# Kernel tuning notes

Measured on AMD Instinct MI355X. Metric: run time of the kernel, lower is better.

The kernel has to match this reference:

```python
import jax, jax.numpy as jnp
import numpy as np

B, L, D, H, UNITS = 64, 1024, 1024, 1024, 1024


def setup_inputs() -> dict:
    key = jax.random.key(0)
    ks = jax.random.split(key, 8)
    s = lambda fan_in: 1.0 / np.sqrt(fan_in)
    return {
        "features": jax.random.normal(ks[0], (B, L, D), jnp.float32),
        "hidden": jax.random.normal(ks[1], (B, H), jnp.float32),
        "W1": jax.random.normal(ks[2], (D, UNITS), jnp.float32) * s(D),
        "b1": jnp.zeros((UNITS,), jnp.float32),
        "W2": jax.random.normal(ks[3], (H, UNITS), jnp.float32) * s(H),
        "b2": jnp.zeros((UNITS,), jnp.float32),
        "V": jax.random.normal(ks[4], (UNITS, 1), jnp.float32) * s(UNITS),
        "bV": jnp.zeros((1,), jnp.float32),
    }


def reference(features, hidden, W1, b1, W2, b2, V, bV):
    # features: [B, L, D], hidden: [B, H]
    proj_f = jnp.einsum("bld,du->blu", features, W1) + b1          # [B, L, U]
    proj_h = (hidden @ W2 + b2)[:, None, :]                         # [B, 1, U]
    score = jnp.tanh(proj_f + proj_h)                               # [B, L, U]
    logits = jnp.einsum("blu,uo->blo", score, V) + bV               # [B, L, 1]
    attention_weights = jax.nn.softmax(logits, axis=1)              # [B, L, 1]
    context_vector = jnp.sum(attention_weights * features, axis=1)  # [B, D]
    return context_vector, attention_weights
```

## Files before the change

kernel.cpp:

```cpp
#include <hip/hip_runtime.h>
#include <hip/hip_bf16.h>
#include <stdint.h>

#define B_ 64
#define L_ 1024
#define D_ 1024
#define U_ 1024
#define M_ (B_ * L_)

typedef __attribute__((ext_vector_type(8))) __bf16 bf16x8;
typedef __attribute__((ext_vector_type(4))) float f32x4;

__device__ __forceinline__ unsigned short f2bf(float f) {
  unsigned u = __float_as_uint(f);
  unsigned r = (u + 0x7fffu + ((u >> 16) & 1u)) >> 16;
  return (unsigned short)r;
}

__device__ __forceinline__ void async_copy16(const void* gptr, void* ldsptr) {
  __builtin_amdgcn_global_load_lds(
      (const __attribute__((address_space(1))) void*)gptr,
      (__attribute__((address_space(3))) void*)ldsptr,
      16, 0, 0);
}

__global__ __launch_bounds__(256) void convert_f_bf16(
    const float4* __restrict__ src, ushort4* __restrict__ dst) {
  long i = (long)blockIdx.x * 256 + threadIdx.x;
  float4 v = src[i];
  ushort4 o;
  o.x = f2bf(v.x); o.y = f2bf(v.y); o.z = f2bf(v.z); o.w = f2bf(v.w);
  dst[i] = o;
}

__global__ __launch_bounds__(256) void transpose_w1(
    const float* __restrict__ W1, unsigned short* __restrict__ W1T) {
  __shared__ float tile[32][33];
  int tx = threadIdx.x & 31, ty = threadIdx.x >> 5;
  int u0 = blockIdx.x * 32, k0 = blockIdx.y * 32;
#pragma unroll
  for (int i = ty; i < 32; i += 8) tile[i][tx] = W1[(long)(k0 + i) * U_ + u0 + tx];
  __syncthreads();
#pragma unroll
  for (int i = ty; i < 32; i += 8)
    W1T[(long)(u0 + i) * D_ + k0 + tx] = f2bf(tile[tx][i]);
}

__global__ __launch_bounds__(256) void proj_h_kernel(
    const float* __restrict__ hidden, const float* __restrict__ W2,
    const float* __restrict__ b1, const float* __restrict__ b2,
    float* __restrict__ ph) {
  int u = blockIdx.x * 256 + threadIdx.x;
  int bbase = blockIdx.y * 8;
  int h0 = blockIdx.z * 512;
  float acc[8];
  float bias = (blockIdx.z == 0) ? (b1[u] + b2[u]) : 0.0f;
#pragma unroll
  for (int i = 0; i < 8; ++i) acc[i] = bias;
  for (int h = h0; h < h0 + 512; ++h) {
    float w = W2[(long)h * U_ + u];
#pragma unroll
    for (int i = 0; i < 8; ++i) acc[i] += hidden[(bbase + i) * 1024 + h] * w;
  }
#pragma unroll
  for (int i = 0; i < 8; ++i) atomicAdd(&ph[(bbase + i) * U_ + u], acc[i]);
}

__global__ __launch_bounds__(256, 2) void fused_score_kernel(
    const unsigned short* __restrict__ A,
    const unsigned short* __restrict__ Bt,
    const float* __restrict__ ph,
    const float* __restrict__ V,
    float* __restrict__ logits) {
  __shared__ unsigned short As[128 * 32];
  __shared__ unsigned short Bs[128 * 32];

  const int tid = threadIdx.x;
  const int wave = tid >> 6;
  const int lane = tid & 63;
  const int l15 = lane & 15;
  const int quad = lane >> 4;
  const int wm = wave >> 1;
  const int wn = wave & 1;
  const long m0 = (long)blockIdx.y * 128;
  const int n0 = blockIdx.x * 128;

  const int srow = lane >> 2;
  const int skof = (lane & 3) * 8;
  const int c0 = wave * 2;
  const unsigned short* Ab = A + (m0 + srow) * 1024 + skof;
  const unsigned short* Bb = Bt + ((long)n0 + srow) * 1024 + skof;

  f32x4 acc[4][4];
#pragma unroll
  for (int i = 0; i < 4; ++i)
#pragma unroll
    for (int j = 0; j < 4; ++j) acc[i][j] = (f32x4){0.f, 0.f, 0.f, 0.f};

  for (int k0 = 0; k0 < 1024; k0 += 32) {
#pragma unroll
    for (int cc = 0; cc < 2; ++cc) {
      const int c = c0 + cc;
      async_copy16(Ab + (long)c * 16 * 1024 + k0, &As[c * 512]);
      async_copy16(Bb + (long)c * 16 * 1024 + k0, &Bs[c * 512]);
    }
    __syncthreads();

    bf16x8 af[4], bf[4];
#pragma unroll
    for (int mi = 0; mi < 4; ++mi)
      af[mi] = *(const bf16x8*)&As[(wm * 64 + mi * 16 + l15) * 32 + quad * 8];
#pragma unroll
    for (int ni = 0; ni < 4; ++ni)
      bf[ni] = *(const bf16x8*)&Bs[(wn * 64 + ni * 16 + l15) * 32 + quad * 8];
#pragma unroll
    for (int mi = 0; mi < 4; ++mi)
#pragma unroll
      for (int ni = 0; ni < 4; ++ni)
        acc[mi][ni] = __builtin_amdgcn_mfma_f32_16x16x32_bf16(
            af[mi], bf[ni], acc[mi][ni], 0, 0, 0);
    __syncthreads();
  }

  const int b = (int)(m0 >> 10);
  float phv[4], vv[4];
#pragma unroll
  for (int ni = 0; ni < 4; ++ni) {
    int u = n0 + wn * 64 + ni * 16 + l15;
    phv[ni] = ph[b * U_ + u];
    vv[ni] = V[u];
  }
#pragma unroll
  for (int mi = 0; mi < 4; ++mi) {
#pragma unroll
    for (int r = 0; r < 4; ++r) {
      float part = 0.f;
#pragma unroll
      for (int ni = 0; ni < 4; ++ni) {
        float s = acc[mi][ni][r] + phv[ni];
        float t = __expf(2.0f * s);
        float th = 1.0f - 2.0f * __builtin_amdgcn_rcpf(t + 1.0f);
        part += th * vv[ni];
      }
      part += __shfl_xor(part, 1, 16);
      part += __shfl_xor(part, 2, 16);
      part += __shfl_xor(part, 4, 16);
      part += __shfl_xor(part, 8, 16);
      if (l15 == 0)
        atomicAdd(&logits[m0 + wm * 64 + mi * 16 + quad * 4 + r], part);
    }
  }
}

__global__ __launch_bounds__(256) void softmax_kernel(
    const float* __restrict__ logits, float* __restrict__ wout) {
  __shared__ float redm[4];
  __shared__ float reds[4];
  int b = blockIdx.x;
  int tid = threadIdx.x;
  int wave = tid >> 6, lane = tid & 63;
  float4 v = *(const float4*)&logits[b * 1024 + tid * 4];
  float m = fmaxf(fmaxf(v.x, v.y), fmaxf(v.z, v.w));
#pragma unroll
  for (int off = 32; off >= 1; off >>= 1) m = fmaxf(m, __shfl_xor(m, off, 64));
  if (lane == 0) redm[wave] = m;
  __syncthreads();
  m = fmaxf(fmaxf(redm[0], redm[1]), fmaxf(redm[2], redm[3]));
  float e0 = __expf(v.x - m), e1 = __expf(v.y - m);
  float e2 = __expf(v.z - m), e3 = __expf(v.w - m);
  float s = e0 + e1 + e2 + e3;
#pragma unroll
  for (int off = 32; off >= 1; off >>= 1) s += __shfl_xor(s, off, 64);
  if (lane == 0) reds[wave] = s;
  __syncthreads();
  s = reds[0] + reds[1] + reds[2] + reds[3];
  float inv = 1.0f / s;
  float4 o = {e0 * inv, e1 * inv, e2 * inv, e3 * inv};
  *(float4*)&wout[b * 1024 + tid * 4] = o;
}

__global__ __launch_bounds__(256) void context_kernel(
    const float* __restrict__ features, const float* __restrict__ wv,
    float* __restrict__ out) {
  int b = blockIdx.x;
  int d = blockIdx.y * 256 + threadIdx.x;
  int l0 = blockIdx.z * 128;
  const float* fp = features + ((long)b * 1024 + l0) * 1024 + d;
  const float* wp = wv + b * 1024 + l0;
  float acc = 0.f;
#pragma unroll 4
  for (int l = 0; l < 128; ++l) acc += wp[l] * fp[(long)l * 1024];
  atomicAdd(&out[b * 1024 + d], acc);
}

extern "C" void kernel_launch(void* const* d_in, const int* in_sizes, int n_in,
                              void* d_out, int out_size, void* d_ws, size_t ws_size,
                              hipStream_t stream) {
  const float* features = (const float*)d_in[0];
  const float* hidden   = (const float*)d_in[1];
  const float* W1       = (const float*)d_in[2];
  const float* b1       = (const float*)d_in[3];
  const float* W2       = (const float*)d_in[4];
  const float* b2       = (const float*)d_in[5];
  const float* V        = (const float*)d_in[6];

  char* ws = (char*)d_ws;
  unsigned short* Fh  = (unsigned short*)ws;
  unsigned short* W1T = (unsigned short*)(ws + 134217728);
  float* ph     = (float*)(ws + 134217728 + 2097152);
  float* logits = (float*)(ws + 134217728 + 2097152 + 262144);
  float* ctx  = (float*)d_out;
  float* wout = (float*)d_out + 65536;

  hipMemsetAsync(ph, 0, 262144 + 262144, stream);
  hipMemsetAsync(d_out, 0, 65536 * sizeof(float), stream);

  convert_f_bf16<<<65536, 256, 0, stream>>>((const float4*)features, (ushort4*)Fh);
  transpose_w1<<<dim3(32, 32), 256, 0, stream>>>(W1, W1T);
  proj_h_kernel<<<dim3(4, 8, 2), 256, 0, stream>>>(hidden, W2, b1, b2, ph);
  fused_score_kernel<<<dim3(8, 512), 256, 0, stream>>>(Fh, W1T, ph, V, logits);
  softmax_kernel<<<64, 256, 0, stream>>>(logits, wout);
  context_kernel<<<dim3(64, 4, 8), 256, 0, stream>>>(features, wout, ctx);
}
```

Measured before the change: 720.9 us.

## Read bf16 features in context kernel, swizzle GEMM tiles, split proj_h wider

The context reduction now reads the bf16 copy of the features, four elements per thread, instead of the fp32 original, which halves that kernel's memory traffic but adds rounding error to the context output. The score GEMM gets a 1D grid with a grouped tile order (8 M-tiles by 8 N-tiles) to improve L2 reuse of A and W1T tiles. proj_h splits the H dimension over 8 chunks instead of 2, giving more blocks for parallelism at the cost of more atomics.

```diff
diff --git a/kernel.cpp b/kernel.cpp
--- a/kernel.cpp
+++ b/kernel.cpp
@@ -15,6 +15,10 @@
   unsigned u = __float_as_uint(f);
   unsigned r = (u + 0x7fffu + ((u >> 16) & 1u)) >> 16;
   return (unsigned short)r;
+}
+
+__device__ __forceinline__ float bf2f(unsigned short h) {
+  return __uint_as_float(((unsigned)h) << 16);
 }
 
 __device__ __forceinline__ void async_copy16(const void* gptr, void* ldsptr) {
@@ -52,12 +56,12 @@
     float* __restrict__ ph) {
   int u = blockIdx.x * 256 + threadIdx.x;
   int bbase = blockIdx.y * 8;
-  int h0 = blockIdx.z * 512;
+  int h0 = blockIdx.z * 128;
   float acc[8];
   float bias = (blockIdx.z == 0) ? (b1[u] + b2[u]) : 0.0f;
 #pragma unroll
   for (int i = 0; i < 8; ++i) acc[i] = bias;
-  for (int h = h0; h < h0 + 512; ++h) {
+  for (int h = h0; h < h0 + 128; ++h) {
     float w = W2[(long)h * U_ + u];
 #pragma unroll
     for (int i = 0; i < 8; ++i) acc[i] += hidden[(bbase + i) * 1024 + h] * w;
@@ -82,8 +86,12 @@
   const int quad = lane >> 4;
   const int wm = wave >> 1;
   const int wn = wave & 1;
-  const long m0 = (long)blockIdx.y * 128;
-  const int n0 = blockIdx.x * 128;
+
+  const int i = blockIdx.x;
+  const int mtile = ((i >> 6) << 3) + (i & 7);
+  const int ntile = (i >> 3) & 7;
+  const long m0 = (long)mtile * 128;
+  const int n0 = ntile * 128;
 
   const int srow = lane >> 2;
   const int skof = (lane & 3) * 8;
@@ -93,9 +101,9 @@
 
   f32x4 acc[4][4];
 #pragma unroll
-  for (int i = 0; i < 4; ++i)
-#pragma unroll
-    for (int j = 0; j < 4; ++j) acc[i][j] = (f32x4){0.f, 0.f, 0.f, 0.f};
+  for (int ii = 0; ii < 4; ++ii)
+#pragma unroll
+    for (int j = 0; j < 4; ++j) acc[ii][j] = (f32x4){0.f, 0.f, 0.f, 0.f};
 
   for (int k0 = 0; k0 < 1024; k0 += 32) {
 #pragma unroll
@@ -180,17 +188,27 @@
 }
 
 __global__ __launch_bounds__(256) void context_kernel(
-    const float* __restrict__ features, const float* __restrict__ wv,
+    const unsigned short* __restrict__ Fh, const float* __restrict__ wv,
     float* __restrict__ out) {
   int b = blockIdx.x;
-  int d = blockIdx.y * 256 + threadIdx.x;
-  int l0 = blockIdx.z * 128;
-  const float* fp = features + ((long)b * 1024 + l0) * 1024 + d;
+  int d4 = threadIdx.x * 4;
+  int l0 = blockIdx.y * 128;
+  const unsigned short* fp = Fh + ((long)b * 1024 + l0) * 1024 + d4;
   const float* wp = wv + b * 1024 + l0;
-  float acc = 0.f;
+  float a0 = 0.f, a1 = 0.f, a2 = 0.f, a3 = 0.f;
 #pragma unroll 4
-  for (int l = 0; l < 128; ++l) acc += wp[l] * fp[(long)l * 1024];
-  atomicAdd(&out[b * 1024 + d], acc);
+  for (int l = 0; l < 128; ++l) {
+    ushort4 f = *(const ushort4*)(fp + (long)l * 1024);
+    float w = wp[l];
+    a0 += w * bf2f(f.x);
+    a1 += w * bf2f(f.y);
+    a2 += w * bf2f(f.z);
+    a3 += w * bf2f(f.w);
+  }
+  atomicAdd(&out[b * 1024 + d4 + 0], a0);
+  atomicAdd(&out[b * 1024 + d4 + 1], a1);
+  atomicAdd(&out[b * 1024 + d4 + 2], a2);
+  atomicAdd(&out[b * 1024 + d4 + 3], a3);
 }
 
 extern "C" void kernel_launch(void* const* d_in, const int* in_sizes, int n_in,
@@ -217,8 +235,8 @@
 
   convert_f_bf16<<<65536, 256, 0, stream>>>((const float4*)features, (ushort4*)Fh);
   transpose_w1<<<dim3(32, 32), 256, 0, stream>>>(W1, W1T);
-  proj_h_kernel<<<dim3(4, 8, 2), 256, 0, stream>>>(hidden, W2, b1, b2, ph);
-  fused_score_kernel<<<dim3(8, 512), 256, 0, stream>>>(Fh, W1T, ph, V, logits);
+  proj_h_kernel<<<dim3(4, 8, 8), 256, 0, stream>>>(hidden, W2, b1, b2, ph);
+  fused_score_kernel<<<4096, 256, 0, stream>>>(Fh, W1T, ph, V, logits);
   softmax_kernel<<<64, 256, 0, stream>>>(logits, wout);
-  context_kernel<<<dim3(64, 4, 8), 256, 0, stream>>>(features, wout, ctx);
-}
+  context_kernel<<<dim3(64, 8), 256, 0, stream>>>(Fh, wout, ctx);
+}
```

After: 596.9 us. -17.2%, faster.
